# Kernel optimization log

Hardware: AMD Instinct MI355X
Metric: run time of the kernel (lower is better)

## Reference

```python
import jax, jax.numpy as jnp
import numpy as np

B, D, O, K = 8192, 256, 256, 16


def setup_inputs() -> dict:
    key = jax.random.key(0)
    k1, k2, k3, k4 = jax.random.split(key, 4)
    x = jax.random.normal(k1, (B, D), dtype=jnp.float32)
    # learned params
    values = jax.random.uniform(k2, (O, D, K), dtype=jnp.float32, minval=-0.05, maxval=0.05)
    skip_w = jax.random.normal(k3, (O, D), dtype=jnp.float32) * (1.0 / np.sqrt(D))
    skip_b = jax.random.uniform(k4, (O,), dtype=jnp.float32, minval=-1.0, maxval=1.0) / np.sqrt(D)
    # fixed buffer (non-trainable)
    grid = jnp.linspace(-1.0, 1.0, K).astype(jnp.float32)
    return {"x": x, "values": values, "skip_w": skip_w, "skip_b": skip_b, "grid": grid}


def reference(x, values, skip_w, skip_b, grid):
    # x: [B, D]; values: [O, D, K]; grid: [K]
    num_knots = grid.shape[0]
    xc = jnp.clip(x, -1.0, 1.0)
    # torch.bucketize(x, grid) (right=False) == searchsorted side='left'
    right = jnp.searchsorted(grid, xc, side="left")            # [B, D]
    left = jnp.clip(right - 1, 0, num_knots - 2)               # [B, D]
    right = left + 1
    g0 = grid[left]
    g1 = grid[right]
    w = (xc - g0) / (g1 - g0 + 1e-12)                          # [B, D]
    # sparse linear-interp coefficients over knots: 2 nonzeros per (b, d)
    coeff = (1.0 - w)[..., None] * jax.nn.one_hot(left, num_knots, dtype=xc.dtype) \
          + w[..., None] * jax.nn.one_hot(right, num_knots, dtype=xc.dtype)  # [B, D, K]
    # y[b,o] = sum_d sum_k coeff[b,d,k] * values[o,d,k]  (== per-dim gather+interp+accumulate)
    y = jnp.einsum("bdk,odk->bo", coeff, values)
    y = y + xc @ skip_w.T + skip_b
    return y
```

## Files before the change

kernel.cpp:

```cpp
#include <hip/hip_runtime.h>
#include <hip/hip_bf16.h>
#include <stdint.h>


#define D_DIM  256
#define O_DIM  256
#define BM     128
#define BK     64
#define NTHR   512

typedef __attribute__((ext_vector_type(8))) short bf16x8;
typedef __attribute__((ext_vector_type(4))) float f32x4;

__global__ __launch_bounds__(256) void kan_prep(
    const float* __restrict__ values,
    const float* __restrict__ skip_w,
    const float* __restrict__ gknots,
    unsigned short* __restrict__ Vp)
{
    int tid = blockIdx.x * blockDim.x + threadIdx.x;
    int e = tid * 8;
    int o = e >> 12;
    int kflat = e & 4095;
    float sw = skip_w[(o << 8) | (kflat >> 4)];
    int kmod = kflat & 15;

    const float4* vp4 = reinterpret_cast<const float4*>(values + e);
    float4 v0 = vp4[0], v1 = vp4[1];
    float f[8] = {v0.x, v0.y, v0.z, v0.w, v1.x, v1.y, v1.z, v1.w};
    unsigned int w[4];
#pragma unroll
    for (int j = 0; j < 4; ++j) {
        float2 ab;
        ab.x = f[2*j]     + gknots[kmod + 2*j]     * sw;
        ab.y = f[2*j + 1] + gknots[kmod + 2*j + 1] * sw;
        __hip_bfloat162 p2 = __float22bfloat162_rn(ab);
        __builtin_memcpy(&w[j], &p2, 4);
    }
    size_t c = (size_t)(kflat >> 3) * 256 + (size_t)o;
    *reinterpret_cast<uint4*>(Vp + c * 8) = make_uint4(w[0], w[1], w[2], w[3]);
}

template<int KS>
__global__ __launch_bounds__(NTHR, 2) void kan_gemm(
    const float* __restrict__ x,
    const unsigned short* __restrict__ Vp,
    float* __restrict__ part)
{
    __shared__ unsigned short As[2][BM * BK];

    constexpr int ITERS = 64 / KS;
    const int t    = threadIdx.x;
    const int lane = t & 63;
    const int wid  = t >> 6;
    const int wm   = wid >> 2;
    const int wn   = wid & 3;
    const int l15  = lane & 15;
    const int lhi  = lane >> 4;

    const int bid = (int)blockIdx.x;
    const int ks  = bid & (KS - 1);
    const int mt  = bid / KS;
    const int bm0 = mt * BM;
    const size_t kc0 = (size_t)ks * (512 / KS);

    const int ar = t >> 2;
    const int ad = t & 3;
    const float* xp = x + (size_t)(bm0 + ar) * D_DIM + ks * (256 / KS) + ad;

    char* arow[2] = { (char*)&As[0][0] + ar * 128, (char*)&As[1][0] + ar * 128 };
    const int ca = ((2 * ad)     ^ (ar & 7)) * 16;
    const int cb = ((2 * ad + 1) ^ (ar & 7)) * 16;

    auto stageA = [&](int buf, float xv) {
        float xc = fminf(1.f, fmaxf(-1.f, xv));
        float tt = (xc + 1.f) * 7.5f;
        int li = (int)tt;
        li = li > 14 ? 14 : li;
        float w1 = tt - (float)li;
        float2 cw; cw.x = 1.f - w1; cw.y = w1;
        __hip_bfloat162 p2 = __float22bfloat162_rn(cw);
        unsigned int pk;
        __builtin_memcpy(&pk, &p2, 4);
        unsigned long long w64 = (unsigned long long)pk << ((li & 1) * 16);
        unsigned int lo = (unsigned int)w64;
        unsigned int hi = (unsigned int)(w64 >> 32);
        int jl = li >> 1;
        unsigned int wd[8];
#pragma unroll
        for (int j = 0; j < 8; ++j)
            wd[j] = (j == jl) ? lo : ((j == jl + 1) ? hi : 0u);
        char* a = arow[buf];
        *reinterpret_cast<uint4*>(a + ca) = make_uint4(wd[0], wd[1], wd[2], wd[3]);
        *reinterpret_cast<uint4*>(a + cb) = make_uint4(wd[4], wd[5], wd[6], wd[7]);
    };

    #define LOADB(BG, KT)                                                      \
        {                                                                      \
            const unsigned short* _b =                                         \
                Vp + (kc0 + (size_t)(KT) * 8) * 2048;                          \
            _Pragma("unroll")                                                  \
            for (int kh = 0; kh < 2; ++kh)                                     \
                _Pragma("unroll")                                              \
                for (int ni = 0; ni < 4; ++ni) {                               \
                    int n = wn * 64 + ni * 16 + l15;                           \
                    BG[kh * 4 + ni] = *reinterpret_cast<const bf16x8*>(        \
                        _b + ((size_t)((kh * 4 + lhi) * 256 + n)) * 8);        \
                }                                                              \
        }

    f32x4 acc[4][4] = {};
    bf16x8 bgA[8], bgB[8];

    int abyte[4], a7[4];
#pragma unroll
    for (int mi = 0; mi < 4; ++mi) {
        int m = wm * 64 + mi * 16 + l15;
        abyte[mi] = m * 128;
        a7[mi] = m & 7;
    }

    float xnxt = xp[0];
    LOADB(bgA, 0);
    stageA(0, xnxt);
    xnxt = (ITERS > 1) ? xp[4] : xnxt;
    asm volatile("s_waitcnt lgkmcnt(0)" ::: "memory");
    __builtin_amdgcn_s_barrier();
    __builtin_amdgcn_sched_barrier(0);

    #define ITERBODY(KT, CUR, BGC, BGN)                                        \
        {                                                                      \
            const bool last = (KT) == ITERS - 1;                               \
            if (!last) LOADB(BGN, (KT) + 1);                                   \
            const char* Ab = (const char*)&As[CUR][0];                         \
            bf16x8 af[4];                                                      \
                                                                   \
            _Pragma("unroll")                                                  \
            for (int mi = 0; mi < 4; ++mi)                                     \
                af[mi] = *reinterpret_cast<const bf16x8*>(                     \
                    Ab + abyte[mi] + ((lhi ^ a7[mi]) << 4));                   \
            _Pragma("unroll")                                                  \
            for (int mi = 0; mi < 4; ++mi)                                     \
                _Pragma("unroll")                                              \
                for (int ni = 0; ni < 4; ++ni)                                 \
                    acc[mi][ni] = __builtin_amdgcn_mfma_f32_16x16x32_bf16(     \
                        af[mi], BGC[ni], acc[mi][ni], 0, 0, 0);                \
                                      \
            if (!last) {                                                       \
                stageA((CUR) ^ 1, xnxt);                                       \
                if ((KT) + 2 < ITERS) xnxt = xp[((KT) + 2) * 4];               \
            }                                                                  \
                                                                   \
            _Pragma("unroll")                                                  \
            for (int mi = 0; mi < 4; ++mi)                                     \
                af[mi] = *reinterpret_cast<const bf16x8*>(                     \
                    Ab + abyte[mi] + (((4 + lhi) ^ a7[mi]) << 4));             \
            _Pragma("unroll")                                                  \
            for (int mi = 0; mi < 4; ++mi)                                     \
                _Pragma("unroll")                                              \
                for (int ni = 0; ni < 4; ++ni)                                 \
                    acc[mi][ni] = __builtin_amdgcn_mfma_f32_16x16x32_bf16(     \
                        af[mi], BGC[4 + ni], acc[mi][ni], 0, 0, 0);            \
            if (!last) {                                                       \
                asm volatile("s_waitcnt lgkmcnt(0)" ::: "memory");             \
                __builtin_amdgcn_s_barrier();                                  \
                __builtin_amdgcn_sched_barrier(0);                             \
            }                                                                  \
        }

    for (int t2 = 0; t2 < ITERS / 2; ++t2) {
        ITERBODY(2 * t2,     0, bgA, bgB);
        ITERBODY(2 * t2 + 1, 1, bgB, bgA);
    }
    #undef ITERBODY
    #undef LOADB

    float* dst = part + (size_t)ks * (8192 * 256);
#pragma unroll
    for (int ni = 0; ni < 4; ++ni) {
        int col = wn * 64 + ni * 16 + l15;
#pragma unroll
        for (int mi = 0; mi < 4; ++mi) {
            f32x4 v = acc[mi][ni];
            int row0 = bm0 + wm * 64 + mi * 16 + lhi * 4;
#pragma unroll
            for (int r = 0; r < 4; ++r)
                dst[(size_t)(row0 + r) * O_DIM + col] = v[r];
        }
    }
}

__global__ __launch_bounds__(256) void kan_reduce(
    const float* __restrict__ part,
    const float* __restrict__ skip_b,
    float* __restrict__ out,
    int nparts)
{
    size_t i4 = (size_t)blockIdx.x * 256 + threadIdx.x;
    size_t e = i4 * 4;
    f32x4 s = *reinterpret_cast<const f32x4*>(&skip_b[e & 255]);
    for (int p = 0; p < nparts; ++p)
        s += *reinterpret_cast<const f32x4*>(part + (size_t)p * (8192 * 256) + e);
    *reinterpret_cast<f32x4*>(out + e) = s;
}

extern "C" void kernel_launch(void* const* d_in, const int* in_sizes, int n_in,
                              void* d_out, int out_size, void* d_ws, size_t ws_size,
                              hipStream_t stream) {
    const float* x      = (const float*)d_in[0];
    const float* values = (const float*)d_in[1];
    const float* skip_w = (const float*)d_in[2];
    const float* skip_b = (const float*)d_in[3];
    const float* gknots = (const float*)d_in[4];
    float* out = (float*)d_out;
    (void)in_sizes; (void)n_in; (void)out_size;

    unsigned short* Vp = (unsigned short*)d_ws;
    float* part = (float*)((char*)d_ws + 2 * 1024 * 1024);

    kan_prep<<<dim3(512), dim3(256), 0, stream>>>(values, skip_w, gknots, Vp);

    const size_t need4 = 2u * 1024 * 1024 + (size_t)4 * 8192 * 256 * 4;
    if (ws_size >= need4) {
        kan_gemm<4><<<dim3(256), dim3(NTHR), 0, stream>>>(x, Vp, part);
        kan_reduce<<<dim3(2048), dim3(256), 0, stream>>>(part, skip_b, out, 4);
    } else {
        kan_gemm<1><<<dim3(64), dim3(NTHR), 0, stream>>>(x, Vp, out);
        kan_reduce<<<dim3(2048), dim3(256), 0, stream>>>(out, skip_b, out, 1);
    }
}
```

Before: 41.43 us.

## Split GEMM output columns across two blocks and raise MFMA wave priority

```diff
diff --git a/kernel.cpp b/kernel.cpp
--- a/kernel.cpp
+++ b/kernel.cpp
@@ -7,7 +7,7 @@
 #define O_DIM  256
 #define BM     128
 #define BK     64
-#define NTHR   512
+#define NTHR   256
 
 typedef __attribute__((ext_vector_type(8))) short bf16x8;
 typedef __attribute__((ext_vector_type(4))) float f32x4;
@@ -53,26 +53,30 @@
     const int t    = threadIdx.x;
     const int lane = t & 63;
     const int wid  = t >> 6;
-    const int wm   = wid >> 2;
-    const int wn   = wid & 3;
+    const int wm   = wid >> 1;
+    const int wn   = wid & 1;
     const int l15  = lane & 15;
     const int lhi  = lane >> 4;
 
     const int bid = (int)blockIdx.x;
     const int ks  = bid & (KS - 1);
-    const int mt  = bid / KS;
+    const int nt  = (bid / KS) & 1;
+    const int mt  = bid / (2 * KS);
     const int bm0 = mt * BM;
+    const int nc0 = nt * 128;
     const size_t kc0 = (size_t)ks * (512 / KS);
 
-    const int ar = t >> 2;
-    const int ad = t & 3;
-    const float* xp = x + (size_t)(bm0 + ar) * D_DIM + ks * (256 / KS) + ad;
+    const int ar  = t >> 1;
+    const int ad2 = (t & 1) * 2;
+    const float* xp = x + (size_t)(bm0 + ar) * D_DIM + ks * (256 / KS) + ad2;
 
     char* arow[2] = { (char*)&As[0][0] + ar * 128, (char*)&As[1][0] + ar * 128 };
-    const int ca = ((2 * ad)     ^ (ar & 7)) * 16;
-    const int cb = ((2 * ad + 1) ^ (ar & 7)) * 16;
-
-    auto stageA = [&](int buf, float xv) {
+    const int cs0 = ((2 * ad2)     ^ (ar & 7)) * 16;
+    const int cs1 = ((2 * ad2 + 1) ^ (ar & 7)) * 16;
+    const int cs2 = ((2 * ad2 + 2) ^ (ar & 7)) * 16;
+    const int cs3 = ((2 * ad2 + 3) ^ (ar & 7)) * 16;
+
+    auto buildwd = [&](float xv, unsigned int* wd) {
         float xc = fminf(1.f, fmaxf(-1.f, xv));
         float tt = (xc + 1.f) * 7.5f;
         int li = (int)tt;
@@ -86,24 +90,30 @@
         unsigned int lo = (unsigned int)w64;
         unsigned int hi = (unsigned int)(w64 >> 32);
         int jl = li >> 1;
-        unsigned int wd[8];
 #pragma unroll
         for (int j = 0; j < 8; ++j)
             wd[j] = (j == jl) ? lo : ((j == jl + 1) ? hi : 0u);
+    };
+
+    auto stageA = [&](int buf, float2 xv) {
+        unsigned int wd[8];
         char* a = arow[buf];
-        *reinterpret_cast<uint4*>(a + ca) = make_uint4(wd[0], wd[1], wd[2], wd[3]);
-        *reinterpret_cast<uint4*>(a + cb) = make_uint4(wd[4], wd[5], wd[6], wd[7]);
+        buildwd(xv.x, wd);
+        *reinterpret_cast<uint4*>(a + cs0) = make_uint4(wd[0], wd[1], wd[2], wd[3]);
+        *reinterpret_cast<uint4*>(a + cs1) = make_uint4(wd[4], wd[5], wd[6], wd[7]);
+        buildwd(xv.y, wd);
+        *reinterpret_cast<uint4*>(a + cs2) = make_uint4(wd[0], wd[1], wd[2], wd[3]);
+        *reinterpret_cast<uint4*>(a + cs3) = make_uint4(wd[4], wd[5], wd[6], wd[7]);
     };
 
     #define LOADB(BG, KT)                                                      \
         {                                                                      \
-            const unsigned short* _b =                                         \
-                Vp + (kc0 + (size_t)(KT) * 8) * 2048;                          \
+            const unsigned short* _b = Vp + (kc0 + (size_t)(KT) * 8) * 2048;   \
             _Pragma("unroll")                                                  \
             for (int kh = 0; kh < 2; ++kh)                                     \
                 _Pragma("unroll")                                              \
                 for (int ni = 0; ni < 4; ++ni) {                               \
-                    int n = wn * 64 + ni * 16 + l15;                           \
+                    int n = nc0 + wn * 64 + ni * 16 + l15;                     \
                     BG[kh * 4 + ni] = *reinterpret_cast<const bf16x8*>(        \
                         _b + ((size_t)((kh * 4 + lhi) * 256 + n)) * 8);        \
                 }                                                              \
@@ -120,52 +130,56 @@
         a7[mi] = m & 7;
     }
 
-    float xnxt = xp[0];
+    float2 x1 = *reinterpret_cast<const float2*>(xp);
     LOADB(bgA, 0);
-    stageA(0, xnxt);
-    xnxt = (ITERS > 1) ? xp[4] : xnxt;
+    float2 xn = (ITERS > 1) ? *reinterpret_cast<const float2*>(xp + 4) : x1;
+    stageA(0, x1);
     asm volatile("s_waitcnt lgkmcnt(0)" ::: "memory");
     __builtin_amdgcn_s_barrier();
     __builtin_amdgcn_sched_barrier(0);
 
-    #define ITERBODY(KT, CUR, BGC, BGN)                                        \
-        {                                                                      \
-            const bool last = (KT) == ITERS - 1;                               \
-            if (!last) LOADB(BGN, (KT) + 1);                                   \
-            const char* Ab = (const char*)&As[CUR][0];                         \
-            bf16x8 af[4];                                                      \
-                                                                   \
-            _Pragma("unroll")                                                  \
-            for (int mi = 0; mi < 4; ++mi)                                     \
-                af[mi] = *reinterpret_cast<const bf16x8*>(                     \
-                    Ab + abyte[mi] + ((lhi ^ a7[mi]) << 4));                   \
-            _Pragma("unroll")                                                  \
-            for (int mi = 0; mi < 4; ++mi)                                     \
-                _Pragma("unroll")                                              \
-                for (int ni = 0; ni < 4; ++ni)                                 \
-                    acc[mi][ni] = __builtin_amdgcn_mfma_f32_16x16x32_bf16(     \
-                        af[mi], BGC[ni], acc[mi][ni], 0, 0, 0);                \
-                                      \
-            if (!last) {                                                       \
-                stageA((CUR) ^ 1, xnxt);                                       \
-                if ((KT) + 2 < ITERS) xnxt = xp[((KT) + 2) * 4];               \
-            }                                                                  \
-                                                                   \
-            _Pragma("unroll")                                                  \
-            for (int mi = 0; mi < 4; ++mi)                                     \
-                af[mi] = *reinterpret_cast<const bf16x8*>(                     \
-                    Ab + abyte[mi] + (((4 + lhi) ^ a7[mi]) << 4));             \
-            _Pragma("unroll")                                                  \
-            for (int mi = 0; mi < 4; ++mi)                                     \
-                _Pragma("unroll")                                              \
-                for (int ni = 0; ni < 4; ++ni)                                 \
-                    acc[mi][ni] = __builtin_amdgcn_mfma_f32_16x16x32_bf16(     \
-                        af[mi], BGC[4 + ni], acc[mi][ni], 0, 0, 0);            \
-            if (!last) {                                                       \
-                asm volatile("s_waitcnt lgkmcnt(0)" ::: "memory");             \
-                __builtin_amdgcn_s_barrier();                                  \
-                __builtin_amdgcn_sched_barrier(0);                             \
-            }                                                                  \
+    #define ITERBODY(KT, CUR, BGC, BGN)                                       \
+        {                                                                     \
+            const bool last = (KT) == ITERS - 1;                              \
+            if (!last) LOADB(BGN, (KT) + 1);                                  \
+            const char* Ab = (const char*)&As[CUR][0];                        \
+            bf16x8 af[4];                                                     \
+                                                                  \
+            _Pragma("unroll")                                                 \
+            for (int mi = 0; mi < 4; ++mi)                                    \
+                af[mi] = *reinterpret_cast<const bf16x8*>(                    \
+                    Ab + abyte[mi] + ((lhi ^ a7[mi]) << 4));                  \
+            __builtin_amdgcn_s_setprio(1);                                    \
+            _Pragma("unroll")                                                 \
+            for (int mi = 0; mi < 4; ++mi)                                    \
+                _Pragma("unroll")                                             \
+                for (int ni = 0; ni < 4; ++ni)                                \
+                    acc[mi][ni] = __builtin_amdgcn_mfma_f32_16x16x32_bf16(    \
+                        af[mi], BGC[ni], acc[mi][ni], 0, 0, 0);               \
+            __builtin_amdgcn_s_setprio(0);                                    \
+            if (!last) {                                                      \
+                stageA((CUR) ^ 1, xn);                                        \
+                if ((KT) + 2 < ITERS)                                         \
+                    xn = *reinterpret_cast<const float2*>(xp + ((KT) + 2) * 4);\
+            }                                                                 \
+                                                                  \
+            _Pragma("unroll")                                                 \
+            for (int mi = 0; mi < 4; ++mi)                                    \
+                af[mi] = *reinterpret_cast<const bf16x8*>(                    \
+                    Ab + abyte[mi] + (((4 + lhi) ^ a7[mi]) << 4));            \
+            __builtin_amdgcn_s_setprio(1);                                    \
+            _Pragma("unroll")                                                 \
+            for (int mi = 0; mi < 4; ++mi)                                    \
+                _Pragma("unroll")                                             \
+                for (int ni = 0; ni < 4; ++ni)                                \
+                    acc[mi][ni] = __builtin_amdgcn_mfma_f32_16x16x32_bf16(    \
+                        af[mi], BGC[4 + ni], acc[mi][ni], 0, 0, 0);           \
+            __builtin_amdgcn_s_setprio(0);                                    \
+            if (!last) {                                                      \
+                asm volatile("s_waitcnt lgkmcnt(0)" ::: "memory");            \
+                __builtin_amdgcn_s_barrier();                                 \
+                __builtin_amdgcn_sched_barrier(0);                            \
+            }                                                                 \
         }
 
     for (int t2 = 0; t2 < ITERS / 2; ++t2) {
@@ -178,7 +192,7 @@
     float* dst = part + (size_t)ks * (8192 * 256);
 #pragma unroll
     for (int ni = 0; ni < 4; ++ni) {
-        int col = wn * 64 + ni * 16 + l15;
+        int col = nc0 + wn * 64 + ni * 16 + l15;
 #pragma unroll
         for (int mi = 0; mi < 4; ++mi) {
             f32x4 v = acc[mi][ni];
@@ -222,10 +236,10 @@
 
     const size_t need4 = 2u * 1024 * 1024 + (size_t)4 * 8192 * 256 * 4;
     if (ws_size >= need4) {
-        kan_gemm<4><<<dim3(256), dim3(NTHR), 0, stream>>>(x, Vp, part);
+        kan_gemm<4><<<dim3(512), dim3(NTHR), 0, stream>>>(x, Vp, part);
         kan_reduce<<<dim3(2048), dim3(256), 0, stream>>>(part, skip_b, out, 4);
     } else {
-        kan_gemm<1><<<dim3(64), dim3(NTHR), 0, stream>>>(x, Vp, out);
+        kan_gemm<1><<<dim3(128), dim3(NTHR), 0, stream>>>(x, Vp, out);
         kan_reduce<<<dim3(2048), dim3(256), 0, stream>>>(out, skip_b, out, 1);
     }
 }
```

Result: no change. 41.50 us (+0.2%).

## Write split-K slice 0 directly to output and remap blocks for L2 locality

Applied to the files above, without the earlier changes.

```diff
diff --git a/kernel.cpp b/kernel.cpp
--- a/kernel.cpp
+++ b/kernel.cpp
@@ -7,6 +7,8 @@
 #define O_DIM  256
 #define BM     128
 #define BK     64
+#define KS     4
+#define ITERS  16
 #define NTHR   512
 
 typedef __attribute__((ext_vector_type(8))) short bf16x8;
@@ -41,15 +43,14 @@
     *reinterpret_cast<uint4*>(Vp + c * 8) = make_uint4(w[0], w[1], w[2], w[3]);
 }
 
-template<int KS>
 __global__ __launch_bounds__(NTHR, 2) void kan_gemm(
     const float* __restrict__ x,
     const unsigned short* __restrict__ Vp,
-    float* __restrict__ part)
+    float* __restrict__ part,
+    float* __restrict__ out)
 {
     __shared__ unsigned short As[2][BM * BK];
 
-    constexpr int ITERS = 64 / KS;
     const int t    = threadIdx.x;
     const int lane = t & 63;
     const int wid  = t >> 6;
@@ -59,14 +60,16 @@
     const int lhi  = lane >> 4;
 
     const int bid = (int)blockIdx.x;
-    const int ks  = bid & (KS - 1);
-    const int mt  = bid / KS;
+    const int m8  = bid & 7;
+    const int ks  = (bid >> 3) & 3;
+    const int mhi = bid >> 5;
+    const int mt  = m8 + 8 * mhi;
     const int bm0 = mt * BM;
-    const size_t kc0 = (size_t)ks * (512 / KS);
+    const size_t kc0 = (size_t)ks * 128;
 
     const int ar = t >> 2;
     const int ad = t & 3;
-    const float* xp = x + (size_t)(bm0 + ar) * D_DIM + ks * (256 / KS) + ad;
+    const float* xp = x + (size_t)(bm0 + ar) * D_DIM + ks * 64 + ad;
 
     char* arow[2] = { (char*)&As[0][0] + ar * 128, (char*)&As[1][0] + ar * 128 };
     const int ca = ((2 * ad)     ^ (ar & 7)) * 16;
@@ -123,7 +126,7 @@
     float xnxt = xp[0];
     LOADB(bgA, 0);
     stageA(0, xnxt);
-    xnxt = (ITERS > 1) ? xp[4] : xnxt;
+    xnxt = xp[4];
     asm volatile("s_waitcnt lgkmcnt(0)" ::: "memory");
     __builtin_amdgcn_s_barrier();
     __builtin_amdgcn_sched_barrier(0);
@@ -139,12 +142,14 @@
             for (int mi = 0; mi < 4; ++mi)                                     \
                 af[mi] = *reinterpret_cast<const bf16x8*>(                     \
                     Ab + abyte[mi] + ((lhi ^ a7[mi]) << 4));                   \
+            __builtin_amdgcn_s_setprio(1);                                     \
             _Pragma("unroll")                                                  \
             for (int mi = 0; mi < 4; ++mi)                                     \
                 _Pragma("unroll")                                              \
                 for (int ni = 0; ni < 4; ++ni)                                 \
                     acc[mi][ni] = __builtin_amdgcn_mfma_f32_16x16x32_bf16(     \
                         af[mi], BGC[ni], acc[mi][ni], 0, 0, 0);                \
+            __builtin_amdgcn_s_setprio(0);                                     \
                                       \
             if (!last) {                                                       \
                 stageA((CUR) ^ 1, xnxt);                                       \
@@ -155,12 +160,14 @@
             for (int mi = 0; mi < 4; ++mi)                                     \
                 af[mi] = *reinterpret_cast<const bf16x8*>(                     \
                     Ab + abyte[mi] + (((4 + lhi) ^ a7[mi]) << 4));             \
+            __builtin_amdgcn_s_setprio(1);                                     \
             _Pragma("unroll")                                                  \
             for (int mi = 0; mi < 4; ++mi)                                     \
                 _Pragma("unroll")                                              \
                 for (int ni = 0; ni < 4; ++ni)                                 \
                     acc[mi][ni] = __builtin_amdgcn_mfma_f32_16x16x32_bf16(     \
                         af[mi], BGC[4 + ni], acc[mi][ni], 0, 0, 0);            \
+            __builtin_amdgcn_s_setprio(0);                                     \
             if (!last) {                                                       \
                 asm volatile("s_waitcnt lgkmcnt(0)" ::: "memory");             \
                 __builtin_amdgcn_s_barrier();                                  \
@@ -175,7 +182,7 @@
     #undef ITERBODY
     #undef LOADB
 
-    float* dst = part + (size_t)ks * (8192 * 256);
+    float* dst = (ks == 0) ? out : part + (size_t)(ks - 1) * (8192 * 256);
 #pragma unroll
     for (int ni = 0; ni < 4; ++ni) {
         int col = wn * 64 + ni * 16 + l15;
@@ -193,15 +200,51 @@
 __global__ __launch_bounds__(256) void kan_reduce(
     const float* __restrict__ part,
     const float* __restrict__ skip_b,
-    float* __restrict__ out,
-    int nparts)
-{
-    size_t i4 = (size_t)blockIdx.x * 256 + threadIdx.x;
-    size_t e = i4 * 4;
-    f32x4 s = *reinterpret_cast<const f32x4*>(&skip_b[e & 255]);
-    for (int p = 0; p < nparts; ++p)
-        s += *reinterpret_cast<const f32x4*>(part + (size_t)p * (8192 * 256) + e);
+    float* __restrict__ out)
+{
+    int rbid = (int)blockIdx.x;
+    int c    = rbid & 7;
+    int tq   = rbid >> 3;
+    int mhi  = tq >> 5;
+    int sub  = tq & 31;
+    int mt   = c + 8 * mhi;
+    int row0 = mt * BM + sub * 4;
+
+    int i   = (int)threadIdx.x;
+    int row = row0 + (i >> 6);
+    int col = (i & 63) * 4;
+    size_t e = (size_t)row * O_DIM + col;
+
+    f32x4 s = *reinterpret_cast<const f32x4*>(out + e);
+    s += *reinterpret_cast<const f32x4*>(skip_b + col);
+    s += *reinterpret_cast<const f32x4*>(part + e);
+    s += *reinterpret_cast<const f32x4*>(part + (size_t)8192 * 256 + e);
+    s += *reinterpret_cast<const f32x4*>(part + (size_t)2 * 8192 * 256 + e);
     *reinterpret_cast<f32x4*>(out + e) = s;
+}
+
+__global__ __launch_bounds__(256) void kan_naive(
+    const float* __restrict__ x,
+    const unsigned short* __restrict__ Vp,
+    const float* __restrict__ skip_b,
+    float* __restrict__ out)
+{
+    int b = blockIdx.x, o = threadIdx.x;
+    float acc = skip_b[o];
+    for (int d = 0; d < 256; ++d) {
+        float xc = fminf(1.f, fmaxf(-1.f, x[(size_t)b * 256 + d]));
+        float tt = (xc + 1.f) * 7.5f;
+        int li = (int)tt; li = li > 14 ? 14 : li;
+        float w1 = tt - (float)li;
+        int k0 = d * 16 + li;
+        unsigned short u0 = Vp[((size_t)(k0 >> 3) * 256 + o) * 8 + (k0 & 7)];
+        int k1 = k0 + 1;
+        unsigned short u1 = Vp[((size_t)(k1 >> 3) * 256 + o) * 8 + (k1 & 7)];
+        float f0 = __uint_as_float((unsigned)u0 << 16);
+        float f1 = __uint_as_float((unsigned)u1 << 16);
+        acc += (1.f - w1) * f0 + w1 * f1;
+    }
+    out[(size_t)b * 256 + o] = acc;
 }
 
 extern "C" void kernel_launch(void* const* d_in, const int* in_sizes, int n_in,
@@ -216,16 +259,16 @@
     (void)in_sizes; (void)n_in; (void)out_size;
 
     unsigned short* Vp = (unsigned short*)d_ws;
-    float* part = (float*)((char*)d_ws + 2 * 1024 * 1024);
+    float* part = (float*)((char*)d_ws + 2u * 1024 * 1024);
 
     kan_prep<<<dim3(512), dim3(256), 0, stream>>>(values, skip_w, gknots, Vp);
 
-    const size_t need4 = 2u * 1024 * 1024 + (size_t)4 * 8192 * 256 * 4;
-    if (ws_size >= need4) {
-        kan_gemm<4><<<dim3(256), dim3(NTHR), 0, stream>>>(x, Vp, part);
-        kan_reduce<<<dim3(2048), dim3(256), 0, stream>>>(part, skip_b, out, 4);
+    const size_t need = 2u * 1024 * 1024
+                      + (size_t)3 * 8192 * 256 * sizeof(float);
+    if (ws_size >= need) {
+        kan_gemm<<<dim3(256), dim3(NTHR), 0, stream>>>(x, Vp, part, out);
+        kan_reduce<<<dim3(2048), dim3(256), 0, stream>>>(part, skip_b, out);
     } else {
-        kan_gemm<1><<<dim3(64), dim3(NTHR), 0, stream>>>(x, Vp, out);
-        kan_reduce<<<dim3(2048), dim3(256), 0, stream>>>(out, skip_b, out, 1);
-    }
-}
+        kan_naive<<<dim3(8192), dim3(256), 0, stream>>>(x, Vp, skip_b, out);
+    }
+}
```

Measured after the change: 41.14 us. About the same (-0.7%).
